# Kernel optimization log

Hardware: AMD Instinct MI355X
Metric: run time of the kernel (lower is better)

The kernel has to match this reference:

```python
import jax, jax.numpy as jnp
import numpy as np

T, B, C = 512, 64, 512
ALPHA = 0.6        # blend coefficient from __init__
TAU = 10.0         # LIF tau
VTH = 1.0          # LIF v_threshold (v_reset = 0, hard reset)
BN_EPS = 1e-5


def spike_fn(x):
    # forward heaviside: spike = (v - v_th >= 0)
    return (x >= 0.0).astype(x.dtype)


def setup_inputs() -> dict:
    key = jax.random.key(0)
    ks = jax.random.split(key, 7)
    x = jax.random.normal(ks[0], (T, B, C), dtype=jnp.float32)
    conv_w = jax.random.normal(ks[1], (C, C, 3), dtype=jnp.float32) / np.sqrt(3.0 * C)
    conv_b = jax.random.normal(ks[2], (C,), dtype=jnp.float32) * 0.01
    bn_gamma = 0.5 + jax.random.uniform(ks[3], (C,), dtype=jnp.float32)
    bn_beta = jax.random.normal(ks[4], (C,), dtype=jnp.float32) * 0.1
    bn_mean = jax.random.normal(ks[5], (C,), dtype=jnp.float32) * 0.1
    bn_var = 0.5 + jax.random.uniform(ks[6], (C,), dtype=jnp.float32)
    return {"x": x, "conv_w": conv_w, "conv_b": conv_b,
            "bn_gamma": bn_gamma, "bn_beta": bn_beta,
            "bn_mean": bn_mean, "bn_var": bn_var}


def reference(x, conv_w, conv_b, bn_gamma, bn_beta, bn_mean, bn_var):
    # x: (T, B, C). Conv1d(k=3, pad=1) on a length-1 sequence reduces to a
    # dense matmul with the middle kernel tap: out = prev @ w[:,:,1].T + b.
    w1 = conv_w[:, :, 1]                      # (C_out, C_in)
    inv_std = bn_gamma * jax.lax.rsqrt(bn_var + BN_EPS)   # fused BN scale
    Bsz, Csz = x.shape[1], x.shape[2]

    def step(carry, x_t):
        prev, v = carry                        # prev: (B, C), v: (B, C) membrane
        conv = jnp.einsum('bc,dc->bd', prev, w1) + conv_b
        bn = (conv - bn_mean) * inv_std + bn_beta
        # LIF (decay_input=True, v_reset=0): v += (x - v) / tau
        v = v + (bn - v) / TAU
        s = spike_fn(v - VTH)
        v = v * (1.0 - s)                      # hard reset to 0
        new = (1.0 - ALPHA) * x_t + ALPHA * s  # alpha blend
        return (new, v), new                   # prev_state detached in torch; no-op for fwd

    init = (jnp.zeros((Bsz, Csz), x.dtype), jnp.zeros((Bsz, Csz), x.dtype))
    _, out = jax.lax.scan(step, init, x)       # out: (T, B, C)
    return out
```

## Files before the change

### kernel.cpp

```cpp
#include <hip/hip_runtime.h>
#include <stdint.h>

#define T_STEPS 512
#define BATCH 64
#define CH 512

using short8 = __attribute__((ext_vector_type(8))) short;
using f32x4  = __attribute__((ext_vector_type(4))) float;

__device__ __forceinline__ unsigned short f2b(float f) {
    union { float f; unsigned u; } c; c.f = f;
    unsigned r = (c.u + 0x7FFFu + ((c.u >> 16) & 1u)) >> 16;
    return (unsigned short)r;
}
__device__ __forceinline__ float b2f(unsigned short h) {
    union { unsigned u; float f; } c; c.u = ((unsigned)h) << 16;
    return c.f;
}

__global__ void prep(const float* __restrict__ cw, const float* __restrict__ cb,
                     const float* __restrict__ gamma, const float* __restrict__ beta,
                     const float* __restrict__ mean, const float* __restrict__ var,
                     unsigned short* __restrict__ wb,
                     float* __restrict__ wt,
                     float* __restrict__ isb,
                     float* __restrict__ k0p,
                     int* __restrict__ flag) {
    int idx = blockIdx.x * 256 + threadIdx.x;
    if (idx == 0) *flag = 0x7fffffff;
    if (idx >= CH * CH) return;
    int d = idx >> 9, c = idx & 511;
    float is = gamma[d] * rsqrtf(var[d] + 1e-5f);
    float w = cw[((size_t)d * CH + c) * 3 + 1];
    wb[idx] = f2b(0.04f * is * w);
    wt[(size_t)c * CH + d] = w;
    if (c == 0) {
        isb[d] = is;
        k0p[d] = 0.1f * ((cb[d] - mean[d]) * is + beta[d]);
    }
}

#define GBM 128
#define GBK 32
#define PADK 40

__global__ __launch_bounds__(512, 2) void gemm_fused(
    const float* __restrict__ Xp,
    const unsigned short* __restrict__ wbp,
    const float* __restrict__ k0p,
    unsigned short* __restrict__ Wbuf,
    float* __restrict__ outp,
    int Mc)
{
    __shared__ __align__(16) unsigned short As[2][GBM][PADK];
    __shared__ __align__(16) unsigned short Bs[2][512][PADK];
    int tid = threadIdx.x;
    int lane = tid & 63, wid = tid >> 6;
    int wm = wid >> 2, wn = wid & 3;
    int i0 = blockIdx.x * GBM;
    int fm = lane & 15, fq = lane >> 4;
    int kq = fq * 8;

    int ar = tid >> 2;
    int ac = (tid & 3) * 8;
    int br = tid >> 2;
    int bc = (tid & 3) * 8;

    float b0e[8];
    #pragma unroll
    for (int j = 0; j < 8; ++j) b0e[j] = k0p[wn * 128 + j * 16 + fm];

    f32x4 acc[4][8] = {};

    int grow = i0 + ar;
    bool arv = grow < Mc;
    int growc = arv ? grow : (Mc - 1);
    const float* xrow = &Xp[(size_t)growc * CH];
    float* orow = &outp[(size_t)grow * CH];

    {
        float4 a0 = *(const float4*)&xrow[ac];
        float4 a1 = *(const float4*)&xrow[ac + 4];
        short8 av;
        av[0]=f2b(a0.x); av[1]=f2b(a0.y); av[2]=f2b(a0.z); av[3]=f2b(a0.w);
        av[4]=f2b(a1.x); av[5]=f2b(a1.y); av[6]=f2b(a1.z); av[7]=f2b(a1.w);
        *(short8*)&As[0][ar][ac] = av;
        #pragma unroll
        for (int p = 0; p < 4; ++p) {
            short8 bv = *(const short8*)&wbp[(size_t)(br + p * 128) * CH + bc];
            *(short8*)&Bs[0][br + p * 128][bc] = bv;
        }
        if (arv) {
            *(float4*)&orow[ac]     = make_float4(0.4f*a0.x, 0.4f*a0.y, 0.4f*a0.z, 0.4f*a0.w);
            *(float4*)&orow[ac + 4] = make_float4(0.4f*a1.x, 0.4f*a1.y, 0.4f*a1.z, 0.4f*a1.w);
        }
    }
    __syncthreads();

    for (int ks = 0; ks < 16; ++ks) {
        int cur = ks & 1;
        int kn = (ks + 1) * GBK;
        float4 na0, na1;
        short8 nb[4];
        if (kn < 512) {
            na0 = *(const float4*)&xrow[kn + ac];
            na1 = *(const float4*)&xrow[kn + ac + 4];
            #pragma unroll
            for (int p = 0; p < 4; ++p)
                nb[p] = *(const short8*)&wbp[(size_t)(br + p * 128) * CH + kn + bc];
        }
        short8 af[4], bfr[8];
        #pragma unroll
        for (int i = 0; i < 4; ++i)
            af[i] = *(const short8*)&As[cur][wm * 64 + i * 16 + fm][kq];
        #pragma unroll
        for (int j = 0; j < 8; ++j)
            bfr[j] = *(const short8*)&Bs[cur][wn * 128 + j * 16 + fm][kq];
        #pragma unroll
        for (int i = 0; i < 4; ++i)
            #pragma unroll
            for (int j = 0; j < 8; ++j)
                acc[i][j] = __builtin_amdgcn_mfma_f32_16x16x32_bf16(af[i], bfr[j], acc[i][j], 0, 0, 0);
        if (kn < 512) {
            short8 av;
            av[0]=f2b(na0.x); av[1]=f2b(na0.y); av[2]=f2b(na0.z); av[3]=f2b(na0.w);
            av[4]=f2b(na1.x); av[5]=f2b(na1.y); av[6]=f2b(na1.z); av[7]=f2b(na1.w);
            *(short8*)&As[cur ^ 1][ar][ac] = av;
            #pragma unroll
            for (int p = 0; p < 4; ++p)
                *(short8*)&Bs[cur ^ 1][br + p * 128][bc] = nb[p];
            if (arv) {
                *(float4*)&orow[kn + ac]     = make_float4(0.4f*na0.x, 0.4f*na0.y, 0.4f*na0.z, 0.4f*na0.w);
                *(float4*)&orow[kn + ac + 4] = make_float4(0.4f*na1.x, 0.4f*na1.y, 0.4f*na1.z, 0.4f*na1.w);
            }
        }
        __syncthreads();
    }

    #pragma unroll
    for (int i = 0; i < 4; ++i)
        #pragma unroll
        for (int r = 0; r < 4; ++r) {
            int row = i0 + wm * 64 + i * 16 + fq * 4 + r;
            if (row < Mc) {
                #pragma unroll
                for (int j = 0; j < 8; ++j) {
                    int col = wn * 128 + j * 16 + fm;
                    Wbuf[(size_t)row * CH + col] = f2b(acc[i][j][r] + b0e[j]);
                }
            }
        }
}

__device__ __forceinline__ short8 wload(const unsigned short* Wbuf, int t, int a0, int b, int c0) {
    int r = t - 1 - a0; if (r < 0) r = 0;
    return *(const short8*)&Wbuf[((size_t)r * BATCH + b) * CH + c0];
}

__global__ __launch_bounds__(64) void scan_a(
    const unsigned short* __restrict__ Wbuf,
    const float* __restrict__ k0p,
    float* __restrict__ Sbuf,
    int t0, int a0, int segs)
{
    int b = blockIdx.x & (BATCH - 1);
    int seg = blockIdx.x >> 6;
    int lane = threadIdx.x, c0 = lane * 8;
    int tstart = t0 + seg * 64;

    float B0[8];
    #pragma unroll
    for (int k = 0; k < 8; ++k) B0[k] = k0p[c0 + k];

    float S[8] = {};
    short8 pz[8];
    #pragma unroll
    for (int p = 0; p < 8; ++p) pz[p] = wload(Wbuf, tstart + p, a0, b, c0);

    for (int ii = 0; ii < 64; ii += 8) {
        #pragma unroll
        for (int p = 0; p < 8; ++p) {
            int t = tstart + ii + p;
            short8 zv = pz[p];
            int tn = ii + p + 8;
            if (tn < 64) pz[p] = wload(Wbuf, tstart + tn, a0, b, c0);
            #pragma unroll
            for (int k = 0; k < 8; ++k) {
                float wv = (t == 0) ? B0[k] : b2f((unsigned short)zv[k]);
                S[k] = fmaf(0.9f, S[k], wv);
            }
        }
    }
    float* sp = &Sbuf[((size_t)b * segs + seg) * CH + c0];
    *(float4*)&sp[0] = make_float4(S[0], S[1], S[2], S[3]);
    *(float4*)&sp[4] = make_float4(S[4], S[5], S[6], S[7]);
}

__global__ __launch_bounds__(64) void scan_c(
    const unsigned short* __restrict__ Wbuf,
    const float* __restrict__ k0p,
    const float* __restrict__ Sbuf,
    const float* __restrict__ vcin,
    float* __restrict__ vcout,
    int* __restrict__ flag,
    int t0, int a0, int segs, int chunk_idx)
{
    const float F = 1.1790184577738595e-3f;
    int b = blockIdx.x & (BATCH - 1);
    int seg = blockIdx.x >> 6;
    int lane = threadIdx.x, c0 = lane * 8;
    int tstart = t0 + seg * 64;

    float B0[8];
    #pragma unroll
    for (int k = 0; k < 8; ++k) B0[k] = k0p[c0 + k];

    float v[8];
    if (t0 == 0) {
        #pragma unroll
        for (int k = 0; k < 8; ++k) v[k] = 0.0f;
    } else {
        const float* vp = &vcin[(size_t)b * CH + c0];
        float4 v0 = *(const float4*)&vp[0], v1 = *(const float4*)&vp[4];
        v[0]=v0.x; v[1]=v0.y; v[2]=v0.z; v[3]=v0.w; v[4]=v1.x; v[5]=v1.y; v[6]=v1.z; v[7]=v1.w;
    }
    for (int s = 0; s < seg; ++s) {
        const float* sp = &Sbuf[((size_t)b * segs + s) * CH + c0];
        float4 s0 = *(const float4*)&sp[0], s1 = *(const float4*)&sp[4];
        float sv[8] = {s0.x, s0.y, s0.z, s0.w, s1.x, s1.y, s1.z, s1.w};
        #pragma unroll
        for (int k = 0; k < 8; ++k) v[k] = fmaf(v[k], F, sv[k]);
    }

    bool anyhit = false;
    short8 pz[8];
    #pragma unroll
    for (int p = 0; p < 8; ++p) pz[p] = wload(Wbuf, tstart + p, a0, b, c0);

    for (int ii = 0; ii < 64; ii += 8) {
        #pragma unroll
        for (int p = 0; p < 8; ++p) {
            int t = tstart + ii + p;
            short8 zv = pz[p];
            int tn = ii + p + 8;
            if (tn < 64) pz[p] = wload(Wbuf, tstart + tn, a0, b, c0);
            float m = -1e30f;
            #pragma unroll
            for (int k = 0; k < 8; ++k) {
                float wv = (t == 0) ? B0[k] : b2f((unsigned short)zv[k]);
                v[k] = fmaf(0.9f, v[k], wv);
                m = fmaxf(m, v[k]);
            }
            anyhit |= (m >= 0.995f);
        }
    }
    if (__ballot(anyhit) != 0ULL && lane == 0) atomicMin(flag, chunk_idx);
    if (seg == segs - 1) {
        float* vp = &vcout[(size_t)b * CH + c0];
        *(float4*)&vp[0] = make_float4(v[0], v[1], v[2], v[3]);
        *(float4*)&vp[4] = make_float4(v[4], v[5], v[6], v[7]);
    }
}

__global__ __launch_bounds__(64) void seq_fix(
    const float* __restrict__ x,
    const float* __restrict__ wt,
    const unsigned short* __restrict__ Wbuf,
    const float* __restrict__ isb,
    const float* __restrict__ k0p,
    const int* __restrict__ flag,
    const float* __restrict__ vcin,
    float* __restrict__ out,
    float* __restrict__ v_state,
    unsigned long long* __restrict__ s_state,
    int t0, int t1, int a0, int chunk_idx, int save_state)
{
    int fl = *flag;
    if (fl > chunk_idx) return;
    int b = blockIdx.x;
    int lane = threadIdx.x;
    int c0 = lane * 8;

    float is6[8], B0[8];
    #pragma unroll
    for (int k = 0; k < 8; ++k) {
        is6[k] = 0.06f * isb[c0 + k];
        B0[k]  = k0p[c0 + k];
    }

    float v[8];
    unsigned long long mk[8];
    if (t0 == 0) {
        #pragma unroll
        for (int k = 0; k < 8; ++k) v[k] = 0.0f;
        #pragma unroll
        for (int j = 0; j < 8; ++j) mk[j] = 0ULL;
    } else if (fl == chunk_idx) {
        #pragma unroll
        for (int k = 0; k < 8; ++k) v[k] = vcin[(size_t)b * CH + c0 + k];
        #pragma unroll
        for (int j = 0; j < 8; ++j) mk[j] = 0ULL;
    } else {
        #pragma unroll
        for (int k = 0; k < 8; ++k) v[k] = v_state[(size_t)b * CH + c0 + k];
        #pragma unroll
        for (int j = 0; j < 8; ++j) mk[j] = s_state[b * 8 + j];
    }

    float xc[8]; short8 wc;
    {
        const float4* xp = (const float4*)&x[((size_t)t0 * BATCH + b) * CH + c0];
        float4 x0 = xp[0], x1 = xp[1];
        xc[0]=x0.x; xc[1]=x0.y; xc[2]=x0.z; xc[3]=x0.w; xc[4]=x1.x; xc[5]=x1.y; xc[6]=x1.z; xc[7]=x1.w;
        wc = wload(Wbuf, t0, a0, b, c0);
    }
    for (int t = t0; t < t1; ++t) {
        float xn[8]; short8 wn_;
        if (t + 1 < t1) {
            const float4* xp = (const float4*)&x[((size_t)(t + 1) * BATCH + b) * CH + c0];
            float4 x0 = xp[0], x1 = xp[1];
            xn[0]=x0.x; xn[1]=x0.y; xn[2]=x0.z; xn[3]=x0.w; xn[4]=x1.x; xn[5]=x1.y; xn[6]=x1.z; xn[7]=x1.w;
            wn_ = wload(Wbuf, t + 1, a0, b, c0);
        }
        float acc[8] = {};
        unsigned long long anym = mk[0]|mk[1]|mk[2]|mk[3]|mk[4]|mk[5]|mk[6]|mk[7];
        if (anym) {
            #pragma unroll
            for (int j = 0; j < 8; ++j) {
                unsigned long long m = mk[j];
                while (m) {
                    int l = __builtin_ctzll(m); m &= m - 1;
                    const float4* wr = (const float4*)&wt[(size_t)(l * 8 + j) * CH + c0];
                    float4 w0 = wr[0], w1 = wr[1];
                    acc[0]+=w0.x; acc[1]+=w0.y; acc[2]+=w0.z; acc[3]+=w0.w;
                    acc[4]+=w1.x; acc[5]+=w1.y; acc[6]+=w1.z; acc[7]+=w1.w;
                }
            }
        }
        bool s[8];
        #pragma unroll
        for (int k = 0; k < 8; ++k) {
            float wv = (t == 0) ? B0[k] : b2f((unsigned short)wc[k]);
            float vv = fmaf(0.9f, v[k], fmaf(is6[k], acc[k], wv));
            s[k] = (vv >= 1.0f);
            v[k] = s[k] ? 0.0f : vv;
        }
        float4* op = (float4*)&out[((size_t)t * BATCH + b) * CH + c0];
        op[0] = make_float4(fmaf(0.4f,xc[0],s[0]?0.6f:0.f), fmaf(0.4f,xc[1],s[1]?0.6f:0.f),
                            fmaf(0.4f,xc[2],s[2]?0.6f:0.f), fmaf(0.4f,xc[3],s[3]?0.6f:0.f));
        op[1] = make_float4(fmaf(0.4f,xc[4],s[4]?0.6f:0.f), fmaf(0.4f,xc[5],s[5]?0.6f:0.f),
                            fmaf(0.4f,xc[6],s[6]?0.6f:0.f), fmaf(0.4f,xc[7],s[7]?0.6f:0.f));
        #pragma unroll
        for (int j = 0; j < 8; ++j) mk[j] = __ballot(s[j]);
        #pragma unroll
        for (int k = 0; k < 8; ++k) xc[k] = xn[k];
        wc = wn_;
    }
    if (save_state) {
        #pragma unroll
        for (int k = 0; k < 8; ++k) v_state[(size_t)b * CH + c0 + k] = v[k];
        if (lane < 8) s_state[b * 8 + lane] = mk[lane];
    }
}

extern "C" void kernel_launch(void* const* d_in, const int* in_sizes, int n_in,
                              void* d_out, int out_size, void* d_ws, size_t ws_size,
                              hipStream_t stream) {
    const float* x     = (const float*)d_in[0];
    const float* cw    = (const float*)d_in[1];
    const float* cb    = (const float*)d_in[2];
    const float* gamma = (const float*)d_in[3];
    const float* beta  = (const float*)d_in[4];
    const float* mean  = (const float*)d_in[5];
    const float* var   = (const float*)d_in[6];
    float* out = (float*)d_out;

    char* ws = (char*)d_ws;
    size_t off = 0;
    auto alloc = [&](size_t bytes) -> char* {
        char* p = ws + off;
        off = (off + bytes + 255) & ~(size_t)255;
        return p;
    };
    unsigned short* wb = (unsigned short*)alloc((size_t)CH * CH * 2);
    float* wt  = (float*)alloc((size_t)CH * CH * 4);
    float* isb = (float*)alloc(CH * 4);
    float* k0p = (float*)alloc(CH * 4);
    int* flag  = (int*)alloc(256);
    float* vst = (float*)alloc((size_t)BATCH * CH * 4);
    unsigned long long* sst = (unsigned long long*)alloc(BATCH * 8 * 8);
    float* vca = (float*)alloc((size_t)BATCH * CH * 4);
    float* vcb = (float*)alloc((size_t)BATCH * CH * 4);
    float* Sb  = (float*)alloc((size_t)BATCH * 8 * CH * 4);
    unsigned short* Wbuf = (unsigned short*)(ws + off);

    size_t avail = (ws_size > off) ? ws_size - off : 0;
    long rows = (long)(avail / ((size_t)BATCH * CH * 2));
    long cs = ((rows - 1) / 64) * 64;
    if (cs > T_STEPS) cs = T_STEPS;
    if (cs < 64) cs = 64;
    int CS = (int)cs;

    hipLaunchKernelGGL(prep, dim3((CH * CH + 255) / 256), dim3(256), 0, stream,
                       cw, cb, gamma, beta, mean, var, wb, wt, isb, k0p, flag);

    float *vin = vca, *vout = vcb;
    int k = 0;
    for (int t0 = 0; t0 < T_STEPS; t0 += CS, ++k) {
        int t1 = t0 + CS; if (t1 > T_STEPS) t1 = T_STEPS;
        int a0 = (t0 == 0) ? 0 : t0 - 1;
        int gend = (t1 == T_STEPS) ? T_STEPS : t1 - 1;
        int Mc = (gend - a0) * BATCH;
        hipLaunchKernelGGL(gemm_fused, dim3((Mc + GBM - 1) / GBM), dim3(512), 0, stream,
                           x + (size_t)a0 * BATCH * CH, wb, k0p, Wbuf,
                           out + (size_t)a0 * BATCH * CH, Mc);
        int segs = (t1 - t0) / 64;
        hipLaunchKernelGGL(scan_a, dim3(64 * segs), dim3(64), 0, stream,
                           Wbuf, k0p, Sb, t0, a0, segs);
        hipLaunchKernelGGL(scan_c, dim3(64 * segs), dim3(64), 0, stream,
                           Wbuf, k0p, Sb, vin, vout, flag, t0, a0, segs, k);
        hipLaunchKernelGGL(seq_fix, dim3(BATCH), dim3(64), 0, stream,
                           x, wt, Wbuf, isb, k0p, flag, vin, out, vst, sst,
                           t0, t1, a0, k, (t1 < T_STEPS) ? 1 : 0);
        float* tmp = vin; vin = vout; vout = tmp;
    }
}
```

Before: 72.80 us.

## Retile fused GEMM to 128x128 blocks with 2D grid and 256 threads

Splits the fused GEMM's N dimension across a second grid axis, so each block computes a 128x128 tile with 4 waves instead of a 128x512 tile with 8 waves. This cuts per-block LDS and accumulator registers, and the launch bounds now target 3 blocks per SM, which raises occupancy and gives more blocks to spread across CUs. The load/store pipeline is restructured into register prefetch with two barriers per K step. The trade-off is that each X row is now loaded and converted to bf16 by four blocks instead of one, and only the blockIdx.y==0 blocks write the scaled output.

```diff
diff --git a/kernel.cpp b/kernel.cpp
--- a/kernel.cpp
+++ b/kernel.cpp
@@ -41,10 +41,10 @@
 }
 
 #define GBM 128
-#define GBK 32
+#define GBN 128
 #define PADK 40
 
-__global__ __launch_bounds__(512, 2) void gemm_fused(
+__global__ __launch_bounds__(256, 3) void gemm_fused(
     const float* __restrict__ Xp,
     const unsigned short* __restrict__ wbp,
     const float* __restrict__ k0p,
@@ -53,90 +53,83 @@
     int Mc)
 {
     __shared__ __align__(16) unsigned short As[2][GBM][PADK];
-    __shared__ __align__(16) unsigned short Bs[2][512][PADK];
+    __shared__ __align__(16) unsigned short Bs[2][GBN][PADK];
     int tid = threadIdx.x;
     int lane = tid & 63, wid = tid >> 6;
-    int wm = wid >> 2, wn = wid & 3;
+    int wm = wid >> 1, wn = wid & 1;
     int i0 = blockIdx.x * GBM;
+    int n0 = blockIdx.y * GBN;
     int fm = lane & 15, fq = lane >> 4;
     int kq = fq * 8;
-
-    int ar = tid >> 2;
-    int ac = (tid & 3) * 8;
-    int br = tid >> 2;
-    int bc = (tid & 3) * 8;
-
-    float b0e[8];
-    #pragma unroll
-    for (int j = 0; j < 8; ++j) b0e[j] = k0p[wn * 128 + j * 16 + fm];
-
-    f32x4 acc[4][8] = {};
+    bool wout = (blockIdx.y == 0);
+
+    int ar = tid >> 1;
+    int ah = (tid & 1) * 16;
 
     int grow = i0 + ar;
     bool arv = grow < Mc;
     int growc = arv ? grow : (Mc - 1);
     const float* xrow = &Xp[(size_t)growc * CH];
+    const unsigned short* brow = &wbp[(size_t)(n0 + ar) * CH + ah];
     float* orow = &outp[(size_t)grow * CH];
 
-    {
-        float4 a0 = *(const float4*)&xrow[ac];
-        float4 a1 = *(const float4*)&xrow[ac + 4];
-        short8 av;
-        av[0]=f2b(a0.x); av[1]=f2b(a0.y); av[2]=f2b(a0.z); av[3]=f2b(a0.w);
-        av[4]=f2b(a1.x); av[5]=f2b(a1.y); av[6]=f2b(a1.z); av[7]=f2b(a1.w);
-        *(short8*)&As[0][ar][ac] = av;
-        #pragma unroll
-        for (int p = 0; p < 4; ++p) {
-            short8 bv = *(const short8*)&wbp[(size_t)(br + p * 128) * CH + bc];
-            *(short8*)&Bs[0][br + p * 128][bc] = bv;
-        }
-        if (arv) {
-            *(float4*)&orow[ac]     = make_float4(0.4f*a0.x, 0.4f*a0.y, 0.4f*a0.z, 0.4f*a0.w);
-            *(float4*)&orow[ac + 4] = make_float4(0.4f*a1.x, 0.4f*a1.y, 0.4f*a1.z, 0.4f*a1.w);
-        }
-    }
-    __syncthreads();
+    float4 ax0 = *(const float4*)&xrow[ah + 0];
+    float4 ax1 = *(const float4*)&xrow[ah + 4];
+    float4 ax2 = *(const float4*)&xrow[ah + 8];
+    float4 ax3 = *(const float4*)&xrow[ah + 12];
+    short8 bv0 = *(const short8*)&brow[0];
+    short8 bv1 = *(const short8*)&brow[8];
+
+    f32x4 acc[4][4] = {};
 
     for (int ks = 0; ks < 16; ++ks) {
         int cur = ks & 1;
-        int kn = (ks + 1) * GBK;
-        float4 na0, na1;
-        short8 nb[4];
+        __syncthreads();
+        {
+            short8 a0, a1;
+            a0[0]=f2b(ax0.x); a0[1]=f2b(ax0.y); a0[2]=f2b(ax0.z); a0[3]=f2b(ax0.w);
+            a0[4]=f2b(ax1.x); a0[5]=f2b(ax1.y); a0[6]=f2b(ax1.z); a0[7]=f2b(ax1.w);
+            a1[0]=f2b(ax2.x); a1[1]=f2b(ax2.y); a1[2]=f2b(ax2.z); a1[3]=f2b(ax2.w);
+            a1[4]=f2b(ax3.x); a1[5]=f2b(ax3.y); a1[6]=f2b(ax3.z); a1[7]=f2b(ax3.w);
+            *(short8*)&As[cur][ar][ah]     = a0;
+            *(short8*)&As[cur][ar][ah + 8] = a1;
+            *(short8*)&Bs[cur][ar][ah]     = bv0;
+            *(short8*)&Bs[cur][ar][ah + 8] = bv1;
+        }
+        __syncthreads();
+        if (wout && arv) {
+            float* o = &orow[ks * 32 + ah];
+            *(float4*)&o[0]  = make_float4(0.4f*ax0.x, 0.4f*ax0.y, 0.4f*ax0.z, 0.4f*ax0.w);
+            *(float4*)&o[4]  = make_float4(0.4f*ax1.x, 0.4f*ax1.y, 0.4f*ax1.z, 0.4f*ax1.w);
+            *(float4*)&o[8]  = make_float4(0.4f*ax2.x, 0.4f*ax2.y, 0.4f*ax2.z, 0.4f*ax2.w);
+            *(float4*)&o[12] = make_float4(0.4f*ax3.x, 0.4f*ax3.y, 0.4f*ax3.z, 0.4f*ax3.w);
+        }
+        int kn = (ks + 1) * 32;
         if (kn < 512) {
-            na0 = *(const float4*)&xrow[kn + ac];
-            na1 = *(const float4*)&xrow[kn + ac + 4];
-            #pragma unroll
-            for (int p = 0; p < 4; ++p)
-                nb[p] = *(const short8*)&wbp[(size_t)(br + p * 128) * CH + kn + bc];
-        }
-        short8 af[4], bfr[8];
+            ax0 = *(const float4*)&xrow[kn + ah + 0];
+            ax1 = *(const float4*)&xrow[kn + ah + 4];
+            ax2 = *(const float4*)&xrow[kn + ah + 8];
+            ax3 = *(const float4*)&xrow[kn + ah + 12];
+            bv0 = *(const short8*)&brow[kn];
+            bv1 = *(const short8*)&brow[kn + 8];
+        }
+        short8 af[4], bf[4];
         #pragma unroll
         for (int i = 0; i < 4; ++i)
             af[i] = *(const short8*)&As[cur][wm * 64 + i * 16 + fm][kq];
         #pragma unroll
-        for (int j = 0; j < 8; ++j)
-            bfr[j] = *(const short8*)&Bs[cur][wn * 128 + j * 16 + fm][kq];
+        for (int j = 0; j < 4; ++j)
+            bf[j] = *(const short8*)&Bs[cur][wn * 64 + j * 16 + fm][kq];
         #pragma unroll
         for (int i = 0; i < 4; ++i)
             #pragma unroll
-            for (int j = 0; j < 8; ++j)
-                acc[i][j] = __builtin_amdgcn_mfma_f32_16x16x32_bf16(af[i], bfr[j], acc[i][j], 0, 0, 0);
-        if (kn < 512) {
-            short8 av;
-            av[0]=f2b(na0.x); av[1]=f2b(na0.y); av[2]=f2b(na0.z); av[3]=f2b(na0.w);
-            av[4]=f2b(na1.x); av[5]=f2b(na1.y); av[6]=f2b(na1.z); av[7]=f2b(na1.w);
-            *(short8*)&As[cur ^ 1][ar][ac] = av;
-            #pragma unroll
-            for (int p = 0; p < 4; ++p)
-                *(short8*)&Bs[cur ^ 1][br + p * 128][bc] = nb[p];
-            if (arv) {
-                *(float4*)&orow[kn + ac]     = make_float4(0.4f*na0.x, 0.4f*na0.y, 0.4f*na0.z, 0.4f*na0.w);
-                *(float4*)&orow[kn + ac + 4] = make_float4(0.4f*na1.x, 0.4f*na1.y, 0.4f*na1.z, 0.4f*na1.w);
-            }
-        }
-        __syncthreads();
-    }
-
+            for (int j = 0; j < 4; ++j)
+                acc[i][j] = __builtin_amdgcn_mfma_f32_16x16x32_bf16(af[i], bf[j], acc[i][j], 0, 0, 0);
+    }
+
+    float b0e[4];
+    #pragma unroll
+    for (int j = 0; j < 4; ++j) b0e[j] = k0p[n0 + wn * 64 + j * 16 + fm];
     #pragma unroll
     for (int i = 0; i < 4; ++i)
         #pragma unroll
@@ -144,8 +137,8 @@
             int row = i0 + wm * 64 + i * 16 + fq * 4 + r;
             if (row < Mc) {
                 #pragma unroll
-                for (int j = 0; j < 8; ++j) {
-                    int col = wn * 128 + j * 16 + fm;
+                for (int j = 0; j < 4; ++j) {
+                    int col = n0 + wn * 64 + j * 16 + fm;
                     Wbuf[(size_t)row * CH + col] = f2b(acc[i][j][r] + b0e[j]);
                 }
             }
@@ -411,7 +404,7 @@
         int a0 = (t0 == 0) ? 0 : t0 - 1;
         int gend = (t1 == T_STEPS) ? T_STEPS : t1 - 1;
         int Mc = (gend - a0) * BATCH;
-        hipLaunchKernelGGL(gemm_fused, dim3((Mc + GBM - 1) / GBM), dim3(512), 0, stream,
+        hipLaunchKernelGGL(gemm_fused, dim3((Mc + GBM - 1) / GBM, 4), dim3(256), 0, stream,
                            x + (size_t)a0 * BATCH * CH, wb, k0p, Wbuf,
                            out + (size_t)a0 * BATCH * CH, Mc);
         int segs = (t1 - t0) / 64;
```

Measured after the change: 90.62 us. 24.5% more time.
